# Optimization experiments

Measured on AMD Instinct MI355X. Metric: run time of the kernel, lower is better.

## Reference

```python
import jax, jax.numpy as jnp
import numpy as np

N, E, A, S = 100000, 1600000, 500000, 50000
F_IN, W, LAYERS = 64, 64, 3


def setup_inputs() -> dict:
    key = jax.random.key(0)
    ks = jax.random.split(key, 20)

    def glorot(k, shape):
        fan_in = shape[-2]
        return jax.random.normal(k, shape, dtype=jnp.float32) / jnp.sqrt(jnp.float32(fan_in))

    return {
        "x": jax.random.normal(ks[0], (N, F_IN), dtype=jnp.float32),
        "edge_src": jax.random.randint(ks[1], (E,), 0, N, dtype=jnp.int32),
        "edge_dst": jax.random.randint(ks[2], (E,), 0, N, dtype=jnp.int32),
        "gather_idx": jax.random.randint(ks[3], (A,), 0, N, dtype=jnp.int32),
        "seg_idx": jax.random.randint(ks[4], (A,), 0, S, dtype=jnp.int32),
        # GraphConv 0: lin_root (no bias) + lin_rel (bias)
        "w_root0": glorot(ks[5], (F_IN, W)),
        "w_rel0": glorot(ks[6], (F_IN, W)),
        "b0": jnp.zeros((W,), jnp.float32),
        # hidden GraphConv layers, stacked
        "w_root_h": glorot(ks[7], (LAYERS - 1, W, W)),
        "w_rel_h": glorot(ks[8], (LAYERS - 1, W, W)),
        "b_h": jnp.zeros((LAYERS - 1, W), jnp.float32),
        # MLP head
        "fc1_w": glorot(ks[9], (W, W)),
        "fc1_b": jnp.zeros((W,), jnp.float32),
        "fc2_w": glorot(ks[10], (W, 32)),
        "fc2_b": jnp.zeros((32,), jnp.float32),
        "fc3_w": glorot(ks[11], (32, 2)),
        "fc3_b": jnp.zeros((2,), jnp.float32),
        "num_sets": S,
    }


def _graph_conv(h, edge_src, edge_dst, w_root, w_rel, b):
    # PyG GraphConv (aggr='add'): out_i = W_root h_i + W_rel * sum_{j->i} h_j + b
    agg = jax.ops.segment_sum(h[edge_src], edge_dst, num_segments=h.shape[0])
    return h @ w_root + agg @ w_rel + b


def reference(x, edge_src, edge_dst, gather_idx, seg_idx,
              w_root0, w_rel0, b0, w_root_h, w_rel_h, b_h,
              fc1_w, fc1_b, fc2_w, fc2_b, fc3_w, fc3_b, num_sets):
    h = jax.nn.elu(_graph_conv(x, edge_src, edge_dst, w_root0, w_rel0, b0))
    for i in range(w_root_h.shape[0]):
        h = jax.nn.elu(_graph_conv(h, edge_src, edge_dst, w_root_h[i], w_rel_h[i], b_h[i]))
    # set pooling: gather node rows then scatter_add into sets
    pooled = jax.ops.segment_sum(h[gather_idx], seg_idx, num_segments=num_sets)  # [S, W]
    h = jax.nn.elu(pooled @ fc1_w + fc1_b)
    # dropout p=0.5 is identity at inference
    h = jax.nn.elu(h @ fc2_w + fc2_b)
    logits = h @ fc3_w + fc3_b
    return jax.nn.log_softmax(logits, axis=1)
```

## Files before the change

kernel.cpp:

```cpp
#include <hip/hip_runtime.h>


#define FEAT 64
#define SH 9
#define BSZ 512
#define CH 512
#define CAP 12288
#define SCHUNK 1024
#define IDXE 256
#define HPAD 8
#define LCHUNK 3200

typedef unsigned short u16;
typedef __attribute__((ext_vector_type(8))) short bf16x8;
typedef __attribute__((ext_vector_type(4))) float f32x4;

__device__ __forceinline__ float bf2f(u16 u) {
  union { unsigned int i; float f; } c; c.i = ((unsigned int)u) << 16; return c.f;
}
__device__ __forceinline__ u16 f2bf(float f) {
  union { float f; unsigned int i; } c; c.f = f;
  unsigned int u = c.i;
  return (u16)((u + 0x7FFFu + ((u >> 16) & 1u)) >> 16);
}

__global__ void p1a2f_kernel(const int* __restrict__ kE, int* __restrict__ cE, int nE, int NBe,
                             const int* __restrict__ kP, int* __restrict__ cP, int nP, int NBp,
                             const float* __restrict__ x, u16* __restrict__ xb, int n4, int g_cvt,
                             const float* __restrict__ wr0, const float* __restrict__ wl0,
                             const float* __restrict__ wrh, const float* __restrict__ wlh,
                             u16* __restrict__ wpack) {
  __shared__ int hist[256];
  int tid = threadIdx.x, b = blockIdx.x;
  if (b < 2 * CH) {
    const int* keys; int* counts; int nK, NB, c;
    if (b < CH) { keys = kE; counts = cE; nK = nE; NB = NBe; c = b; }
    else        { keys = kP; counts = cP; nK = nP; NB = NBp; c = b - CH; }
    hist[tid] = 0;
    __syncthreads();
    int len = (nK + CH - 1) / CH;
    int cbeg = c * len, cend = min(nK, cbeg + len);
    for (int i = cbeg + tid; i < cend; i += 256) atomicAdd(&hist[keys[i] >> SH], 1);
    __syncthreads();
    if (tid < NB) counts[tid * CH + c] = hist[tid];
  } else if (b < 2 * CH + g_cvt) {
    int i = (b - 2 * CH) * 256 + tid;
    if (i < n4) {
      float4 v = ((const float4*)x)[i];
      ushort4 o = { f2bf(v.x), f2bf(v.y), f2bf(v.z), f2bf(v.w) };
      ((ushort4*)xb)[i] = o;
    }
  } else {
    int t4 = (b - 2 * CH - g_cvt) * 4 + (tid >> 6);
    if (t4 < 48) {
      int l = t4 >> 4, t = t4 & 15;
      int kt = t >> 2, nt = t & 3;
      int lane = tid & 63;
      const float* wr; const float* wl;
      if (l == 0) { wr = wr0; wl = wl0; }
      else        { wr = wrh + (l - 1) * FEAT * FEAT; wl = wlh + (l - 1) * FEAT * FEAT; }
      int n = nt * 16 + (lane & 15);
      int k0 = kt * 32 + (lane >> 4) * 8;
      u16* dst = wpack + (((size_t)l * 16 + t) * 64 + lane) * 8;
#pragma unroll
      for (int j = 0; j < 8; ++j) {
        int k = k0 + j;
        float v = (k < FEAT) ? wr[k * FEAT + n] : wl[(k - FEAT) * FEAT + n];
        dst[j] = f2bf(v);
      }
    } else if (t4 == 48) {
      int lane = tid & 63;
      if (lane < 16) {
        int Nn = n4 >> 4;
        ushort4 z = {0, 0, 0, 0};
        ((ushort4*)(xb + (size_t)Nn * FEAT))[lane] = z;
      }
    }
  }
}

__global__ void scan1_kernel(int* __restrict__ d0, int* __restrict__ bs0, int L0, int nb0,
                             int* __restrict__ d1, int* __restrict__ bs1, int L1) {
  __shared__ int tsum[256];
  int tid = threadIdx.x, b = blockIdx.x;
  int* data; int* bsums; int L, c;
  if (b < nb0) { data = d0; bsums = bs0; L = L0; c = b; }
  else         { data = d1; bsums = bs1; L = L1; c = b - nb0; }
  int base = c * SCHUNK + tid * 4;
  int v[4];
#pragma unroll
  for (int i = 0; i < 4; ++i) v[i] = (base + i < L) ? data[base + i] : 0;
  int local = v[0] + v[1] + v[2] + v[3];
  tsum[tid] = local;
  __syncthreads();
  for (int off = 1; off < 256; off <<= 1) {
    int u = (tid >= off) ? tsum[tid - off] : 0;
    __syncthreads();
    tsum[tid] += u;
    __syncthreads();
  }
  int excl = tsum[tid] - local;
  if (tid == 255) bsums[c] = tsum[255];
  int run = excl;
#pragma unroll
  for (int i = 0; i < 4; ++i) {
    if (base + i < L) data[base + i] = run;
    run += v[i];
  }
}

__global__ void scan3_kernel(int* __restrict__ d0, const int* __restrict__ bs0,
                             int* __restrict__ bb0, int L0, int NB0, int tot0, int nb0, int g0,
                             int* __restrict__ d1, const int* __restrict__ bs1,
                             int* __restrict__ bb1, int L1, int NB1, int tot1, int nb1) {
  __shared__ int t[256];
  int b = blockIdx.x, tid = threadIdx.x;
  int* data; const int* bsums; int* bbase; int L, NB, tot, nb, i;
  if (b < g0) { data = d0; bsums = bs0; bbase = bb0; L = L0; NB = NB0; tot = tot0; nb = nb0; i = b * 256 + tid; }
  else        { data = d1; bsums = bs1; bbase = bb1; L = L1; NB = NB1; tot = tot1; nb = nb1; i = (b - g0) * 256 + tid; }
  int v = (tid < nb) ? bsums[tid] : 0;
  t[tid] = v;
  __syncthreads();
  for (int off = 1; off < 256; off <<= 1) {
    int u = (tid >= off) ? t[tid - off] : 0;
    __syncthreads();
    t[tid] += u;
    __syncthreads();
  }
  int incl = t[tid];
  __syncthreads();
  t[tid] = incl - v;
  __syncthreads();
  if (i < L) {
    int val = data[i] + t[i / SCHUNK];
    data[i] = val;
    if ((i & (CH - 1)) == 0) bbase[i / CH] = val;
  }
  if (i == 0) bbase[NB] = tot;
}

__global__ void __launch_bounds__(256)
p1b2_kernel(const int* __restrict__ s0, const int* __restrict__ k0,
            const int* __restrict__ c0, int* __restrict__ bin0, int n0, int NB0,
            const int* __restrict__ s1, const int* __restrict__ k1,
            const int* __restrict__ c1, int* __restrict__ bin1, int n1, int NB1) {
  __shared__ int s_bin[LCHUNK];
  __shared__ unsigned char s_bu[LCHUNK];
  __shared__ int lcur[256];
  __shared__ int gdiff[256];
  __shared__ int ts[256];
  int tid = threadIdx.x, b = blockIdx.x;
  const int* src; const int* keys; const int* counts; int* bin; int nE, NB, c;
  if (b < CH) { src = s0; keys = k0; counts = c0; bin = bin0; nE = n0; NB = NB0; c = b; }
  else        { src = s1; keys = k1; counts = c1; bin = bin1; nE = n1; NB = NB1; c = b - CH; }
  int len = (nE + CH - 1) / CH;
  int cbeg = c * len, cend = min(nE, cbeg + len);
  int L = cend - cbeg;

  int cur = 0, v = 0;
  if (tid < NB) {
    int f = tid * CH + c;
    cur = counts[f];
    int nxt = (f + 1 < NB * CH) ? counts[f + 1] : nE;
    v = nxt - cur;
  }
  ts[tid] = v;
  __syncthreads();
  for (int off = 1; off < 256; off <<= 1) {
    int u = (tid >= off) ? ts[tid - off] : 0;
    __syncthreads();
    ts[tid] += u;
    __syncthreads();
  }
  int excl = ts[tid] - v;
  lcur[tid] = excl;
  gdiff[tid] = cur - excl;
  __syncthreads();

  if (L <= LCHUNK) {
    for (int i = cbeg + tid; i < cend; i += 256) {
      int k = keys[i];
      int bu = k >> SH;
      int pos = atomicAdd(&lcur[bu], 1);
      s_bin[pos] = (src[i] << SH) | (k & (BSZ - 1));
      s_bu[pos] = (unsigned char)bu;
    }
    __syncthreads();
    for (int i = tid; i < L; i += 256) {
      int bu = s_bu[i];
      bin[gdiff[bu] + i] = s_bin[i];
    }
  } else {
    for (int i = cbeg + tid; i < cend; i += 256) {
      int k = keys[i];
      int bu = k >> SH;
      int pos = atomicAdd(&lcur[bu], 1);
      bin[gdiff[bu] + pos] = (src[i] << SH) | (k & (BSZ - 1));
    }
  }
}

__global__ void __launch_bounds__(256) p2_kernel(const int* __restrict__ bin0,
                                                 const int* __restrict__ bb0,
                                                 int* __restrict__ csr0, int* __restrict__ rs0,
                                                 int nn0, int NB0,
                                                 const int* __restrict__ bin1,
                                                 const int* __restrict__ bb1,
                                                 int* __restrict__ csr1, int* __restrict__ rs1,
                                                 int nn1) {
  __shared__ int s_csr[CAP];
  __shared__ int hist[BSZ];
  __shared__ int excl[BSZ];
  __shared__ int ts[256];
  int tid = threadIdx.x, bb = blockIdx.x;
  const int* bin; const int* bbase; int* csr; int* rs; int n_nodes, b;
  if (bb < NB0) { bin = bin0; bbase = bb0; csr = csr0; rs = rs0; n_nodes = nn0; b = bb; }
  else          { bin = bin1; bbase = bb1; csr = csr1; rs = rs1; n_nodes = nn1; b = bb - NB0; }
  int base = bbase[b];
  int cnt = bbase[b + 1] - base;
  int node_lo = b * BSZ;
  int nnode = min(BSZ, n_nodes - node_lo);

  hist[tid] = 0; hist[tid + 256] = 0;
  __syncthreads();
  for (int i = tid; i < cnt; i += 256) atomicAdd(&hist[bin[base + i] & (BSZ - 1)], 1);
  __syncthreads();

  int a0 = hist[2 * tid], a1 = hist[2 * tid + 1];
  int pair = a0 + a1;
  ts[tid] = pair;
  __syncthreads();
  for (int off = 1; off < 256; off <<= 1) {
    int u = (tid >= off) ? ts[tid - off] : 0;
    __syncthreads();
    ts[tid] += u;
    __syncthreads();
  }
  int pexcl = ts[tid] - pair;
  excl[2 * tid] = pexcl;
  excl[2 * tid + 1] = pexcl + a0;
  __syncthreads();

  for (int t = tid; t < nnode; t += 256) rs[node_lo + t] = base + excl[t];
  if (tid == 0 && node_lo + nnode >= n_nodes) rs[n_nodes] = bbase[(n_nodes + BSZ - 1) / BSZ];
  hist[tid] = excl[tid]; hist[tid + 256] = excl[tid + 256];
  __syncthreads();

  if (cnt <= CAP) {
    for (int i = tid; i < cnt; i += 256) {
      int e = bin[base + i];
      int pos = atomicAdd(&hist[e & (BSZ - 1)], 1);
      s_csr[pos] = e >> SH;
    }
    __syncthreads();
    for (int i = tid; i < cnt; i += 256) csr[base + i] = s_csr[i];
  } else {
    for (int i = tid; i < cnt; i += 256) {
      int e = bin[base + i];
      int pos = atomicAdd(&hist[e & (BSZ - 1)], 1);
      csr[base + pos] = e >> SH;
    }
  }
}

__device__ __forceinline__ float4 reduce_sub(float4 a) {
  a.x += __shfl_xor(a.x, 16, 64); a.y += __shfl_xor(a.y, 16, 64);
  a.z += __shfl_xor(a.z, 16, 64); a.w += __shfl_xor(a.w, 16, 64);
  a.x += __shfl_xor(a.x, 32, 64); a.y += __shfl_xor(a.y, 32, 64);
  a.z += __shfl_xor(a.z, 32, 64); a.w += __shfl_xor(a.w, 32, 64);
  return a;
}

struct RowB { ushort4 a, b, c, e; };

__device__ __forceinline__ RowB load_b16(const u16* __restrict__ hb, const int* idx,
                                         int i, int d, int ch, int sent) {
  int j0 = idx[i], j1 = idx[i + 4], j2 = idx[i + 8], j3 = idx[i + 12];
  j0 = (i      < d) ? j0 : sent;
  j1 = (i + 4  < d) ? j1 : sent;
  j2 = (i + 8  < d) ? j2 : sent;
  j3 = (i + 12 < d) ? j3 : sent;
  RowB r;
  r.a = ((const ushort4*)(hb + (size_t)((unsigned)(j0 * FEAT))))[ch];
  r.b = ((const ushort4*)(hb + (size_t)((unsigned)(j1 * FEAT))))[ch];
  r.c = ((const ushort4*)(hb + (size_t)((unsigned)(j2 * FEAT))))[ch];
  r.e = ((const ushort4*)(hb + (size_t)((unsigned)(j3 * FEAT))))[ch];
  return r;
}

__device__ __forceinline__ float4 acc_b16(float4 acc, RowB r) {
  acc.x += (bf2f(r.a.x) + bf2f(r.b.x)) + (bf2f(r.c.x) + bf2f(r.e.x));
  acc.y += (bf2f(r.a.y) + bf2f(r.b.y)) + (bf2f(r.c.y) + bf2f(r.e.y));
  acc.z += (bf2f(r.a.z) + bf2f(r.b.z)) + (bf2f(r.c.z) + bf2f(r.e.z));
  acc.w += (bf2f(r.a.w) + bf2f(r.b.w)) + (bf2f(r.c.w) + bf2f(r.e.w));
  return acc;
}

template <class FW>
__device__ __forceinline__ void gather8(const u16* __restrict__ hb,
                                        const int* __restrict__ rs,
                                        const int* __restrict__ csr,
                                        int* sidx, int wbase, int n, int sent,
                                        int sub, int ch, int lane, FW&& wr) {
  int r[9];
#pragma unroll
  for (int j = 0; j < 9; ++j) r[j] = rs[min(wbase + j, n)];
  int rbeg = r[0];
  int run = r[8] - rbeg;
  const int* eb;
  if (run <= IDXE) {
    for (int i = lane; i < run; i += 64) sidx[i] = csr[rbeg + i];
    eb = sidx;
  } else {
    eb = csr + rbeg;
  }
  int nt = min(8, n - wbase);
  if (nt == 8) {
    RowB fn = load_b16(hb, eb, sub, r[1] - r[0], ch, sent);
#pragma unroll
    for (int t = 0; t < 8; ++t) {
      int off = r[t] - rbeg;
      int d = r[t + 1] - r[t];
      RowB cur = fn;
      if (t < 7) fn = load_b16(hb, eb + (r[t + 1] - rbeg), sub, r[t + 2] - r[t + 1], ch, sent);
      float4 acc = {0.f, 0.f, 0.f, 0.f};
      for (int i = sub + 16; i < d; i += 16) {
        RowB nx = load_b16(hb, eb + off, i, d, ch, sent);
        acc = acc_b16(acc, cur);
        cur = nx;
      }
      acc = acc_b16(acc, cur);
      wr(t, reduce_sub(acc));
    }
  } else {
    for (int t = 0; t < nt; ++t) {
      int off = r[t] - rbeg;
      int d = r[t + 1] - r[t];
      float4 acc = {0.f, 0.f, 0.f, 0.f};
      for (int i = sub; i < d; i += 16)
        acc = acc_b16(acc, load_b16(hb, eb + off, i, d, ch, sent));
      wr(t, reduce_sub(acc));
    }
  }
}

__global__ void __launch_bounds__(256, 8)
layer_fused_kernel(const u16* __restrict__ hb,
                   const int* __restrict__ rs,
                   const int* __restrict__ csr,
                   const u16* __restrict__ wpack,
                   const float* __restrict__ bias,
                   u16* __restrict__ outb, int n) {
  __shared__ u16 s_h[32][FEAT + HPAD];
  __shared__ u16 s_a[32][FEAT + HPAD];
  __shared__ int s_idx[4][IDXE + 16];
  const int tid = threadIdx.x;
  const int wv = __builtin_amdgcn_readfirstlane(tid >> 6);
  const int lane = tid & 63;
  const int sub = lane >> 4;
  const int ch = lane & 15;
  const int base = blockIdx.x * 32;

  for (int it = 0; it < 2; ++it) {
    int idx = tid + it * 256;
    int nl = idx >> 4, c = idx & 15;
    int node = base + nl;
    if (node < n)
      *(ushort4*)&s_h[nl][c * 4] = ((const ushort4*)(hb + (size_t)node * FEAT))[c];
  }

  int wbase = base + wv * 8;
  if (wbase < n) {
    gather8(hb, rs, csr, &s_idx[wv][0], wbase, n, n, sub, ch, lane,
            [&](int t, float4 acc) {
              if (sub == 0) {
                ushort4 o = { f2bf(acc.x), f2bf(acc.y), f2bf(acc.z), f2bf(acc.w) };
                *(ushort4*)&s_a[wv * 8 + t][ch * 4] = o;
              }
            });
  }
  __syncthreads();

  const int mt = wv & 1;
  const int ntb = (wv >> 1) * 2;
  const int mrow = mt * 16 + (lane & 15);
  const int koff = (lane >> 4) * 8;
  f32x4 acc0 = {0.f, 0.f, 0.f, 0.f};
  f32x4 acc1 = {0.f, 0.f, 0.f, 0.f};
#pragma unroll
  for (int kt = 0; kt < 4; ++kt) {
    bf16x8 a;
    if (kt < 2) a = *(const bf16x8*)&s_h[mrow][kt * 32 + koff];
    else        a = *(const bf16x8*)&s_a[mrow][(kt - 2) * 32 + koff];
    bf16x8 b0 = *(const bf16x8*)&wpack[(((size_t)kt * 4 + ntb) * 64 + lane) * 8];
    bf16x8 b1 = *(const bf16x8*)&wpack[(((size_t)kt * 4 + ntb + 1) * 64 + lane) * 8];
    acc0 = __builtin_amdgcn_mfma_f32_16x16x32_bf16(a, b0, acc0, 0, 0, 0);
    acc1 = __builtin_amdgcn_mfma_f32_16x16x32_bf16(a, b1, acc1, 0, 0, 0);
  }
  __syncthreads();

  const int col = lane & 15;
  const int rbase = (lane >> 4) * 4;
  const float bs0 = bias[ntb * 16 + col];
  const float bs1 = bias[(ntb + 1) * 16 + col];
#pragma unroll
  for (int rg = 0; rg < 4; ++rg) {
    int nl = mt * 16 + rbase + rg;
    float v0 = acc0[rg] + bs0;
    float v1 = acc1[rg] + bs1;
    v0 = v0 > 0.f ? v0 : (__expf(v0) - 1.f);
    v1 = v1 > 0.f ? v1 : (__expf(v1) - 1.f);
    s_h[nl][ntb * 16 + col] = f2bf(v0);
    s_h[nl][(ntb + 1) * 16 + col] = f2bf(v1);
  }
  __syncthreads();

  for (int it = 0; it < 2; ++it) {
    int idx = tid + it * 256;
    int nl = idx >> 4, c = idx & 15;
    int node = base + nl;
    if (node < n)
      ((ushort4*)(outb + (size_t)node * FEAT))[c] = *(const ushort4*)&s_h[nl][c * 4];
  }

  if (blockIdx.x == 0 && tid < 16) {
    ushort4 z = {0, 0, 0, 0};
    ((ushort4*)(outb + (size_t)n * FEAT))[tid] = z;
  }
}

__global__ void __launch_bounds__(512)
pool_mlp_kernel(const u16* __restrict__ hb,
                const int* __restrict__ rs,
                const int* __restrict__ csr,
                const float* __restrict__ fc1_w, const float* __restrict__ fc1_b,
                const float* __restrict__ fc2_w, const float* __restrict__ fc2_b,
                const float* __restrict__ fc3_w, const float* __restrict__ fc3_b,
                float* __restrict__ out, int nsets, int nnodes) {
  __shared__ float s_p[64][FEAT + 4];
  __shared__ int s_idx[8][IDXE + 16];
  const int tid = threadIdx.x;
  const int wv = __builtin_amdgcn_readfirstlane(tid >> 6);
  const int lane = tid & 63;
  const int sub = lane >> 4;
  const int ch = lane & 15;
  const int base = blockIdx.x * 64;

  int wbase = base + wv * 8;
  if (wbase < nsets) {
    gather8(hb, rs, csr, &s_idx[wv][0], wbase, nsets, nnodes, sub, ch, lane,
            [&](int t, float4 acc) {
              if (sub == 0) *(float4*)&s_p[wv * 8 + t][ch * 4] = acc;
            });
  }
  __syncthreads();

  {
    const int jb = wv * 8;
    float acc[8];
#pragma unroll
    for (int jj = 0; jj < 8; ++jj) acc[jj] = fc1_b[jb + jj];
    for (int k = 0; k < FEAT; k += 4) {
      const float4 pv = *(const float4*)&s_p[lane][k];
      const float pk[4] = {pv.x, pv.y, pv.z, pv.w};
#pragma unroll
      for (int kk = 0; kk < 4; ++kk) {
        const float* w = fc1_w + (k + kk) * FEAT + jb;
#pragma unroll
        for (int jj = 0; jj < 8; ++jj) acc[jj] += pk[kk] * w[jj];
      }
    }
    __syncthreads();
#pragma unroll
    for (int jj = 0; jj < 8; ++jj) {
      float a = acc[jj];
      s_p[lane][jb + jj] = a > 0.f ? a : (__expf(a) - 1.f);
    }
  }
  __syncthreads();

  {
    const int jb = wv * 4;
    float acc[4];
#pragma unroll
    for (int jj = 0; jj < 4; ++jj) acc[jj] = fc2_b[jb + jj];
    for (int k = 0; k < FEAT; k += 4) {
      const float4 tv = *(const float4*)&s_p[lane][k];
      const float tk[4] = {tv.x, tv.y, tv.z, tv.w};
#pragma unroll
      for (int kk = 0; kk < 4; ++kk) {
        const float* w = fc2_w + (k + kk) * 32 + jb;
#pragma unroll
        for (int jj = 0; jj < 4; ++jj) acc[jj] += tk[kk] * w[jj];
      }
    }
    __syncthreads();
#pragma unroll
    for (int jj = 0; jj < 4; ++jj) {
      float a = acc[jj];
      s_p[lane][jb + jj] = a > 0.f ? a : (__expf(a) - 1.f);
    }
  }
  __syncthreads();

  if (wv == 0) {
    int s = base + lane;
    if (s < nsets) {
      float a0 = fc3_b[0], a1 = fc3_b[1];
      for (int k = 0; k < 32; k += 4) {
        const float4 tv = *(const float4*)&s_p[lane][k];
        const float tk[4] = {tv.x, tv.y, tv.z, tv.w};
#pragma unroll
        for (int kk = 0; kk < 4; ++kk) {
          a0 += tk[kk] * fc3_w[(k + kk) * 2 + 0];
          a1 += tk[kk] * fc3_w[(k + kk) * 2 + 1];
        }
      }
      float m = fmaxf(a0, a1);
      float lse = m + logf(__expf(a0 - m) + __expf(a1 - m));
      float2 r = {a0 - lse, a1 - lse};
      *(float2*)(out + (size_t)s * 2) = r;
    }
  }
}

extern "C" void kernel_launch(void* const* d_in, const int* in_sizes, int n_in,
                              void* d_out, int out_size, void* d_ws, size_t ws_size,
                              hipStream_t stream) {
  const float* x        = (const float*)d_in[0];
  const int* edge_src   = (const int*)d_in[1];
  const int* edge_dst   = (const int*)d_in[2];
  const int* gather_idx = (const int*)d_in[3];
  const int* seg_idx    = (const int*)d_in[4];
  const float* w_root0  = (const float*)d_in[5];
  const float* w_rel0   = (const float*)d_in[6];
  const float* b0       = (const float*)d_in[7];
  const float* w_root_h = (const float*)d_in[8];
  const float* w_rel_h  = (const float*)d_in[9];
  const float* b_h      = (const float*)d_in[10];
  const float* fc1_w    = (const float*)d_in[11];
  const float* fc1_b    = (const float*)d_in[12];
  const float* fc2_w    = (const float*)d_in[13];
  const float* fc2_b    = (const float*)d_in[14];
  const float* fc3_w    = (const float*)d_in[15];
  const float* fc3_b    = (const float*)d_in[16];

  const int N = in_sizes[0] / FEAT;
  const int E = in_sizes[1];
  const int A = in_sizes[3];
  const int S = out_size / 2;

  const int NB_e = (N + BSZ - 1) / BSZ;
  const int NB_p = (S + BSZ - 1) / BSZ;
  const int L_e = NB_e * CH, L_p = NB_p * CH;
  const int nb_e = (L_e + SCHUNK - 1) / SCHUNK;
  const int nb_p = (L_p + SCHUNK - 1) / SCHUNK;
  const int g_e = (L_e + 255) / 256, g_p = (L_p + 255) / 256;

  size_t hrow_bytes = (size_t)(N + 1) * FEAT * sizeof(u16);
  char* ws = (char*)d_ws;
  size_t off = 0;
  auto alloc = [&](size_t bytes) { void* p = ws + off; off += (bytes + 15) & ~(size_t)15; return p; };
  u16* xb       = (u16*)alloc(hrow_bytes);
  u16* b1b      = (u16*)alloc(hrow_bytes);
  u16* b2b      = (u16*)alloc(hrow_bytes);
  int* csr_e    = (int*)alloc((size_t)(E + 16) * 4);
  int* bin_e    = (int*)alloc((size_t)E * 4);
  int* rs_e     = (int*)alloc((size_t)(N + 1) * 4);
  int* counts_e = (int*)alloc((size_t)L_e * 4);
  int* bbase_e  = (int*)alloc((size_t)(NB_e + 1) * 4);
  int* csr_p    = (int*)alloc((size_t)(A + 16) * 4);
  int* bin_p    = (int*)alloc((size_t)A * 4);
  int* rs_p     = (int*)alloc((size_t)(S + 1) * 4);
  int* counts_p = (int*)alloc((size_t)L_p * 4);
  int* bbase_p  = (int*)alloc((size_t)(NB_p + 1) * 4);
  int* bsums_e  = (int*)alloc(256 * 4);
  int* bsums_p  = (int*)alloc(256 * 4);
  u16* wpack    = (u16*)alloc((size_t)3 * 16 * 64 * 8 * sizeof(u16));

  dim3 blk(256);
  dim3 blk512(512);

  int n4 = N * FEAT / 4;
  int g_cvt = (n4 + 255) / 256;
  int g_pp = 13;

  p1a2f_kernel<<<2 * CH + g_cvt + g_pp, blk, 0, stream>>>(
      edge_dst, counts_e, E, NB_e, seg_idx, counts_p, A, NB_p,
      x, xb, n4, g_cvt, w_root0, w_rel0, w_root_h, w_rel_h, wpack);
  scan1_kernel<<<nb_e + nb_p, blk, 0, stream>>>(counts_e, bsums_e, L_e, nb_e,
                                                counts_p, bsums_p, L_p);
  scan3_kernel<<<g_e + g_p, blk, 0, stream>>>(counts_e, bsums_e, bbase_e, L_e, NB_e, E, nb_e, g_e,
                                              counts_p, bsums_p, bbase_p, L_p, NB_p, A, nb_p);
  p1b2_kernel<<<2 * CH, blk, 0, stream>>>(edge_src, edge_dst, counts_e, bin_e, E, NB_e,
                                          gather_idx, seg_idx, counts_p, bin_p, A, NB_p);
  p2_kernel<<<NB_e + NB_p, blk, 0, stream>>>(bin_e, bbase_e, csr_e, rs_e, N, NB_e,
                                             bin_p, bbase_p, csr_p, rs_p, S);

  int lgrid = (N + 31) / 32;
  int pgrid = (S + 63) / 64;

  layer_fused_kernel<<<lgrid, blk, 0, stream>>>(xb, rs_e, csr_e, wpack,
                                                b0, b1b, N);
  layer_fused_kernel<<<lgrid, blk, 0, stream>>>(b1b, rs_e, csr_e, wpack + 16 * 64 * 8,
                                                b_h, b2b, N);
  layer_fused_kernel<<<lgrid, blk, 0, stream>>>(b2b, rs_e, csr_e, wpack + 2 * 16 * 64 * 8,
                                                b_h + FEAT, b1b, N);

  pool_mlp_kernel<<<pgrid, blk512, 0, stream>>>(b1b, rs_p, csr_p,
                                                fc1_w, fc1_b, fc2_w, fc2_b, fc3_w, fc3_b,
                                                (float*)d_out, S, N);
}
```

Measured before the change: 280.7 us.

## Gather neighbor features from fp8 copies of node embeddings

Adds fp8 (e4m3) shadow copies of the node feature tables, written alongside the bf16 outputs in the conversion and layer kernels. The edge aggregation gather now reads 64-byte fp8 rows instead of 128-byte bf16 rows, which halves the random-access traffic of the dominant gather. In exchange it adds extra stores per layer and noticeably lowers the precision of the aggregated neighbor sums.

Result: faster. 271.2 us (-3.4%).

```diff
diff --git a/kernel.cpp b/kernel.cpp
--- a/kernel.cpp
+++ b/kernel.cpp
@@ -12,8 +12,10 @@
 #define LCHUNK 3200
 
 typedef unsigned short u16;
+typedef unsigned char u8;
 typedef __attribute__((ext_vector_type(8))) short bf16x8;
 typedef __attribute__((ext_vector_type(4))) float f32x4;
+typedef __attribute__((ext_vector_type(2))) float f32x2;
 
 __device__ __forceinline__ float bf2f(u16 u) {
   union { unsigned int i; float f; } c; c.i = ((unsigned int)u) << 16; return c.f;
@@ -24,9 +26,21 @@
   return (u16)((u + 0x7FFFu + ((u >> 16) & 1u)) >> 16);
 }
 
+__device__ __forceinline__ unsigned pack_fp8x4(float a, float b, float c, float d) {
+  int lo = __builtin_amdgcn_cvt_pk_fp8_f32(a, b, 0, 0);
+  return (unsigned)__builtin_amdgcn_cvt_pk_fp8_f32(c, d, lo, 1);
+}
+__device__ __forceinline__ float4 unpack_fp8x4(unsigned v) {
+  f32x2 lo = __builtin_amdgcn_cvt_pk_f32_fp8(v, 0);
+  f32x2 hi = __builtin_amdgcn_cvt_pk_f32_fp8(v, 1);
+  float4 r; r.x = lo.x; r.y = lo.y; r.z = hi.x; r.w = hi.y;
+  return r;
+}
+
 __global__ void p1a2f_kernel(const int* __restrict__ kE, int* __restrict__ cE, int nE, int NBe,
                              const int* __restrict__ kP, int* __restrict__ cP, int nP, int NBp,
-                             const float* __restrict__ x, u16* __restrict__ xb, int n4, int g_cvt,
+                             const float* __restrict__ x, u16* __restrict__ xb,
+                             u8* __restrict__ xb8, int n4, int g_cvt,
                              const float* __restrict__ wr0, const float* __restrict__ wl0,
                              const float* __restrict__ wrh, const float* __restrict__ wlh,
                              u16* __restrict__ wpack) {
@@ -49,6 +63,7 @@
       float4 v = ((const float4*)x)[i];
       ushort4 o = { f2bf(v.x), f2bf(v.y), f2bf(v.z), f2bf(v.w) };
       ((ushort4*)xb)[i] = o;
+      ((unsigned*)xb8)[i] = pack_fp8x4(v.x, v.y, v.z, v.w);
     }
   } else {
     int t4 = (b - 2 * CH - g_cvt) * 4 + (tid >> 6);
@@ -70,10 +85,12 @@
       }
     } else if (t4 == 48) {
       int lane = tid & 63;
+      int Nn = n4 >> 4;
       if (lane < 16) {
-        int Nn = n4 >> 4;
         ushort4 z = {0, 0, 0, 0};
         ((ushort4*)(xb + (size_t)Nn * FEAT))[lane] = z;
+      } else if (lane < 32) {
+        ((unsigned*)(xb8 + (size_t)Nn * FEAT))[lane & 15] = 0u;
       }
     }
   }
@@ -344,13 +361,90 @@
   }
 }
 
+struct Row8 { unsigned a, b, c, e; };
+
+__device__ __forceinline__ Row8 load_b8(const u8* __restrict__ h8, const int* idx,
+                                        int i, int d, int ch, int sent) {
+  int j0 = idx[i], j1 = idx[i + 4], j2 = idx[i + 8], j3 = idx[i + 12];
+  j0 = (i      < d) ? j0 : sent;
+  j1 = (i + 4  < d) ? j1 : sent;
+  j2 = (i + 8  < d) ? j2 : sent;
+  j3 = (i + 12 < d) ? j3 : sent;
+  Row8 r;
+  r.a = ((const unsigned*)(h8 + (size_t)((unsigned)(j0 * FEAT))))[ch];
+  r.b = ((const unsigned*)(h8 + (size_t)((unsigned)(j1 * FEAT))))[ch];
+  r.c = ((const unsigned*)(h8 + (size_t)((unsigned)(j2 * FEAT))))[ch];
+  r.e = ((const unsigned*)(h8 + (size_t)((unsigned)(j3 * FEAT))))[ch];
+  return r;
+}
+
+__device__ __forceinline__ float4 acc_b8(float4 acc, Row8 r) {
+  float4 A = unpack_fp8x4(r.a), B = unpack_fp8x4(r.b);
+  float4 C = unpack_fp8x4(r.c), E = unpack_fp8x4(r.e);
+  acc.x += (A.x + B.x) + (C.x + E.x);
+  acc.y += (A.y + B.y) + (C.y + E.y);
+  acc.z += (A.z + B.z) + (C.z + E.z);
+  acc.w += (A.w + B.w) + (C.w + E.w);
+  return acc;
+}
+
+template <class FW>
+__device__ __forceinline__ void gather8q(const u8* __restrict__ h8,
+                                         const int* __restrict__ rs,
+                                         const int* __restrict__ csr,
+                                         int* sidx, int wbase, int n, int sent,
+                                         int sub, int ch, int lane, FW&& wr) {
+  int r[9];
+#pragma unroll
+  for (int j = 0; j < 9; ++j) r[j] = rs[min(wbase + j, n)];
+  int rbeg = r[0];
+  int run = r[8] - rbeg;
+  const int* eb;
+  if (run <= IDXE) {
+    for (int i = lane; i < run; i += 64) sidx[i] = csr[rbeg + i];
+    eb = sidx;
+  } else {
+    eb = csr + rbeg;
+  }
+  int nt = min(8, n - wbase);
+  if (nt == 8) {
+    Row8 fn = load_b8(h8, eb, sub, r[1] - r[0], ch, sent);
+#pragma unroll
+    for (int t = 0; t < 8; ++t) {
+      int off = r[t] - rbeg;
+      int d = r[t + 1] - r[t];
+      Row8 cur = fn;
+      if (t < 7) fn = load_b8(h8, eb + (r[t + 1] - rbeg), sub, r[t + 2] - r[t + 1], ch, sent);
+      float4 acc = {0.f, 0.f, 0.f, 0.f};
+      for (int i = sub + 16; i < d; i += 16) {
+        Row8 nx = load_b8(h8, eb + off, i, d, ch, sent);
+        acc = acc_b8(acc, cur);
+        cur = nx;
+      }
+      acc = acc_b8(acc, cur);
+      wr(t, reduce_sub(acc));
+    }
+  } else {
+    for (int t = 0; t < nt; ++t) {
+      int off = r[t] - rbeg;
+      int d = r[t + 1] - r[t];
+      float4 acc = {0.f, 0.f, 0.f, 0.f};
+      for (int i = sub; i < d; i += 16)
+        acc = acc_b8(acc, load_b8(h8, eb + off, i, d, ch, sent));
+      wr(t, reduce_sub(acc));
+    }
+  }
+}
+
 __global__ void __launch_bounds__(256, 8)
 layer_fused_kernel(const u16* __restrict__ hb,
+                   const u8* __restrict__ g8,
                    const int* __restrict__ rs,
                    const int* __restrict__ csr,
                    const u16* __restrict__ wpack,
                    const float* __restrict__ bias,
-                   u16* __restrict__ outb, int n) {
+                   u16* __restrict__ outb,
+                   u8* __restrict__ out8, int n) {
   __shared__ u16 s_h[32][FEAT + HPAD];
   __shared__ u16 s_a[32][FEAT + HPAD];
   __shared__ int s_idx[4][IDXE + 16];
@@ -371,13 +465,13 @@
 
   int wbase = base + wv * 8;
   if (wbase < n) {
-    gather8(hb, rs, csr, &s_idx[wv][0], wbase, n, n, sub, ch, lane,
-            [&](int t, float4 acc) {
-              if (sub == 0) {
-                ushort4 o = { f2bf(acc.x), f2bf(acc.y), f2bf(acc.z), f2bf(acc.w) };
-                *(ushort4*)&s_a[wv * 8 + t][ch * 4] = o;
-              }
-            });
+    gather8q(g8, rs, csr, &s_idx[wv][0], wbase, n, n, sub, ch, lane,
+             [&](int t, float4 acc) {
+               if (sub == 0) {
+                 ushort4 o = { f2bf(acc.x), f2bf(acc.y), f2bf(acc.z), f2bf(acc.w) };
+                 *(ushort4*)&s_a[wv * 8 + t][ch * 4] = o;
+               }
+             });
   }
   __syncthreads();
 
@@ -419,13 +513,19 @@
     int idx = tid + it * 256;
     int nl = idx >> 4, c = idx & 15;
     int node = base + nl;
-    if (node < n)
-      ((ushort4*)(outb + (size_t)node * FEAT))[c] = *(const ushort4*)&s_h[nl][c * 4];
+    if (node < n) {
+      ushort4 v = *(const ushort4*)&s_h[nl][c * 4];
+      ((ushort4*)(outb + (size_t)node * FEAT))[c] = v;
+      if (out8)
+        ((unsigned*)(out8 + (size_t)node * FEAT))[c] =
+            pack_fp8x4(bf2f(v.x), bf2f(v.y), bf2f(v.z), bf2f(v.w));
+    }
   }
 
   if (blockIdx.x == 0 && tid < 16) {
     ushort4 z = {0, 0, 0, 0};
     ((ushort4*)(outb + (size_t)n * FEAT))[tid] = z;
+    if (out8) ((unsigned*)(out8 + (size_t)n * FEAT))[tid] = 0u;
   }
 }
 
@@ -558,12 +658,16 @@
   const int g_e = (L_e + 255) / 256, g_p = (L_p + 255) / 256;
 
   size_t hrow_bytes = (size_t)(N + 1) * FEAT * sizeof(u16);
+  size_t h8_bytes   = (size_t)(N + 1) * FEAT;
   char* ws = (char*)d_ws;
   size_t off = 0;
   auto alloc = [&](size_t bytes) { void* p = ws + off; off += (bytes + 15) & ~(size_t)15; return p; };
   u16* xb       = (u16*)alloc(hrow_bytes);
   u16* b1b      = (u16*)alloc(hrow_bytes);
   u16* b2b      = (u16*)alloc(hrow_bytes);
+  u8* xb8       = (u8*)alloc(h8_bytes);
+  u8* h8a       = (u8*)alloc(h8_bytes);
+  u8* h8b       = (u8*)alloc(h8_bytes);
   int* csr_e    = (int*)alloc((size_t)(E + 16) * 4);
   int* bin_e    = (int*)alloc((size_t)E * 4);
   int* rs_e     = (int*)alloc((size_t)(N + 1) * 4);
@@ -587,7 +691,7 @@
 
   p1a2f_kernel<<<2 * CH + g_cvt + g_pp, blk, 0, stream>>>(
       edge_dst, counts_e, E, NB_e, seg_idx, counts_p, A, NB_p,
-      x, xb, n4, g_cvt, w_root0, w_rel0, w_root_h, w_rel_h, wpack);
+      x, xb, xb8, n4, g_cvt, w_root0, w_rel0, w_root_h, w_rel_h, wpack);
   scan1_kernel<<<nb_e + nb_p, blk, 0, stream>>>(counts_e, bsums_e, L_e, nb_e,
                                                 counts_p, bsums_p, L_p);
   scan3_kernel<<<g_e + g_p, blk, 0, stream>>>(counts_e, bsums_e, bbase_e, L_e, NB_e, E, nb_e, g_e,
@@ -600,12 +704,12 @@
   int lgrid = (N + 31) / 32;
   int pgrid = (S + 63) / 64;
 
-  layer_fused_kernel<<<lgrid, blk, 0, stream>>>(xb, rs_e, csr_e, wpack,
-                                                b0, b1b, N);
-  layer_fused_kernel<<<lgrid, blk, 0, stream>>>(b1b, rs_e, csr_e, wpack + 16 * 64 * 8,
-                                                b_h, b2b, N);
-  layer_fused_kernel<<<lgrid, blk, 0, stream>>>(b2b, rs_e, csr_e, wpack + 2 * 16 * 64 * 8,
-                                                b_h + FEAT, b1b, N);
+  layer_fused_kernel<<<lgrid, blk, 0, stream>>>(xb, xb8, rs_e, csr_e, wpack,
+                                                b0, b1b, h8a, N);
+  layer_fused_kernel<<<lgrid, blk, 0, stream>>>(b1b, h8a, rs_e, csr_e, wpack + 16 * 64 * 8,
+                                                b_h, b2b, h8b, N);
+  layer_fused_kernel<<<lgrid, blk, 0, stream>>>(b2b, h8b, rs_e, csr_e, wpack + 2 * 16 * 64 * 8,
+                                                b_h + FEAT, b1b, (u8*)nullptr, N);
 
   pool_mlp_kernel<<<pgrid, blk512, 0, stream>>>(b1b, rs_p, csr_p,
                                                 fc1_w, fc1_b, fc2_w, fc2_b, fc3_w, fc3_b,
```
